# Kernel tuning notes

Hardware: AMD Instinct MI355X
Metric: run time of the kernel (lower is better)

The kernel has to match this reference:

```python
import jax, jax.numpy as jnp
import numpy as np

N_FEAT = 1024
NEG_INF = -1e30  # stand-in for -inf that is safe in fp32 softmax


def setup_inputs() -> dict:
    key = jax.random.key(0)
    k1, k2 = jax.random.split(key)
    T, C = 4096, N_FEAT
    x = jax.random.normal(k1, (T, C), dtype=jnp.float32)
    W = jax.random.normal(k2, (C, 3 * C), dtype=jnp.float32) * (1.0 / np.sqrt(C))
    b = jnp.zeros((3 * C,), dtype=jnp.float32)
    return {"x": x, "W": W, "b": b, "n_padd": 0}


def reference(x, W, b, n_padd):
    T, C = x.shape
    qkv = x @ W + b                      # [T, 3C]
    q, k, v = jnp.split(qkv, 3, axis=1)  # each [T, C]
    att = (q @ k.T) * (1.0 / jnp.sqrt(jnp.float32(C)))  # [T, T]
    idx = jnp.arange(T)
    # causal mask AND padding mask: only keys >= n_padd for queries >= n_padd
    mask = (idx[None, :] <= idx[:, None]) & (idx[None, :] >= n_padd) & (idx[:, None] >= n_padd)
    att = jnp.where(mask, att, NEG_INF)
    att = jax.nn.softmax(att, axis=-1)
    y = att @ v                          # [T, C]
    return y
```

## Files before the change

### kernel.cpp

```cpp
#include <hip/hip_runtime.h>
#include <hip/hip_bf16.h>
#include <math.h>

#define C_DIM 1024
#define QKS  2048

typedef __attribute__((ext_vector_type(8))) short bf16x8;
typedef __attribute__((ext_vector_type(4))) float f32x4;

__device__ __forceinline__ unsigned short f2bf(float f) {
  __hip_bfloat16 h = __float2bfloat16(f);
  return *(reinterpret_cast<unsigned short*>(&h));
}
__device__ __forceinline__ float bf2f(unsigned short u) {
  return __uint_as_float(((unsigned int)u) << 16);
}
__device__ __forceinline__ f32x4 mfma16(bf16x8 a, bf16x8 b, f32x4 c) {
  return __builtin_amdgcn_mfma_f32_16x16x32_bf16(a, b, c, 0, 0, 0);
}
__device__ __forceinline__ void gload_lds16(const unsigned short* g,
                                            unsigned short* l) {
  __builtin_amdgcn_global_load_lds(
      (const __attribute__((address_space(1))) void*)(g),
      (__attribute__((address_space(3))) void*)(l), 16, 0, 0);
}

#define VMCNT(n)  asm volatile("s_waitcnt vmcnt(" #n ")" ::: "memory")
#define LGKMCNT0  asm volatile("s_waitcnt lgkmcnt(0)" ::: "memory")
#define SBAR      __builtin_amdgcn_sched_barrier(0)
#define BARRIER   __builtin_amdgcn_s_barrier()

__global__ __launch_bounds__(256) void prep(
    const float* __restrict__ x, const float* __restrict__ W,
    unsigned short* __restrict__ xb, unsigned short* __restrict__ WT, int nc) {
  __shared__ float Ls[64][65];
  const int id = (int)blockIdx.x;
  if (id < nc) {
    const int i = (id * 256 + threadIdx.x) << 2;
    float4 v = *(const float4*)(x + i);
    ushort4 u;
    u.x = f2bf(v.x); u.y = f2bf(v.y); u.z = f2bf(v.z); u.w = f2bf(v.w);
    *(ushort4*)(xb + i) = u;
    return;
  }
  const int id2 = id - nc;
  const int n0 = (id2 % 48) * 64;
  const int k0 = (id2 / 48) * 64;
  const int c = (threadIdx.x & 15) << 2;
  const int r = threadIdx.x >> 4;
#pragma unroll
  for (int rr = 0; rr < 64; rr += 16) {
    float4 v = *(const float4*)(W + (size_t)(k0 + r + rr) * 3072 + n0 + c);
    Ls[r + rr][c + 0] = v.x; Ls[r + rr][c + 1] = v.y;
    Ls[r + rr][c + 2] = v.z; Ls[r + rr][c + 3] = v.w;
  }
  __syncthreads();
#pragma unroll
  for (int rr = 0; rr < 64; rr += 16) {
    const int X = r + rr;
    ushort4 u;
    u.x = f2bf(Ls[c + 0][X]); u.y = f2bf(Ls[c + 1][X]);
    u.z = f2bf(Ls[c + 2][X]); u.w = f2bf(Ls[c + 3][X]);
    *(ushort4*)(WT + (size_t)(n0 + X) * C_DIM + k0 + c) = u;
  }
}

template <int MODE>
__global__ __launch_bounds__(512) void gemm256(
    const unsigned short* __restrict__ A_, const unsigned short* __restrict__ BT_,
    void* __restrict__ Cv, const float* __restrict__ bias_,
    int lda, int ldb, int ldc, int T) {
  __shared__ __align__(16) unsigned short As[2][2][128][64];
  __shared__ __align__(16) unsigned short Bs[2][2][128][64];

  const int tid = threadIdx.x, lane = tid & 63, w = tid >> 6;
  const int wr = w >> 2, wc = w & 3;
  const int qd = lane >> 4, n16 = lane & 15;

  const unsigned short* A  = A_;
  const unsigned short* BT = BT_;
  const float* bias = bias_;
  unsigned short* Cb = (unsigned short*)Cv;
  float* Cf = (float*)Cv;
  int ldc_ = ldc;
  int m0, n0, kbeg = 0, kend = C_DIM;
  bool use_atomic = false, rowbias = false;

  if (MODE == 4) {
    const int nQKx = QKS >> 8;
    const int nQK  = (T >> 8) * nQKx;
    int id = (int)blockIdx.x;
    if (id < nQK) {
      m0 = (id / nQKx) << 8; n0 = (id % nQKx) << 8;
    } else {
      id -= nQK;
      const int nVx = T >> 8;
      m0 = (id / nVx) << 8; n0 = (id % nVx) << 8;
      A  = BT_ + (size_t)QKS * C_DIM;
      BT = A_;
      Cb = (unsigned short*)Cv + (size_t)T * QKS;
      bias = bias_ + QKS; rowbias = true; ldc_ = T;
    }
  } else if (MODE == 2) {
    if ((int)blockIdx.x > (int)blockIdx.y) return;
    m0 = (int)blockIdx.y << 8; n0 = (int)blockIdx.x << 8;
  } else {
    const int nnx = C_DIM >> 8;
    int id = (int)blockIdx.x;
    const int nx = id % nnx;
    int s = id / nnx;
    int bi = 0;
    while (s >= ((bi >> 2) + 1)) { s -= (bi >> 2) + 1; ++bi; }
    m0 = bi << 8; n0 = nx << 8;
    kbeg = s << 10;
    const int kfull = (bi + 1) << 8;
    kend = kbeg + 1024 < kfull ? kbeg + 1024 : kfull;
    use_atomic = (kfull > 1024);
  }

  const int NT = (kend - kbeg) >> 6;

  const int l3 = lane >> 3;
  const int su = (((lane & 7) ^ l3) << 3);
  const unsigned short* asrc[2][2];
  const unsigned short* bsrc[2][2];
#pragma unroll
  for (int g = 0; g < 2; ++g)
#pragma unroll
    for (int c = 0; c < 2; ++c) {
      asrc[g][c] = A  + (size_t)(m0 + c * 128 + g * 64 + (w << 3) + l3) * lda + kbeg + su;
      bsrc[g][c] = BT + (size_t)(n0 + (c * 2 + (w >> 2)) * 64 + g * 32 + ((w & 3) << 3) + l3) * ldb + kbeg + su;
    }

#define STAGE_A(buf, g, kk) do { \
    gload_lds16(asrc[g][0] + (kk), &As[buf][g][(w << 3)][0]);      \
    gload_lds16(asrc[g][1] + (kk), &As[buf][g][64 + (w << 3)][0]); \
  } while (0)
#define STAGE_B(buf, g, kk) do { \
    gload_lds16(bsrc[g][0] + (kk), &Bs[buf][g][(w << 3)][0]);      \
    gload_lds16(bsrc[g][1] + (kk), &Bs[buf][g][64 + (w << 3)][0]); \
  } while (0)

  const int arow = (wr << 6) + n16;
  const int brow = (wc << 5) + n16;
  const int sw0 = ((qd ^ (n16 & 7)) << 3);
  const int sw1 = (((4 + qd) ^ (n16 & 7)) << 3);

#define READ_A(AA, mh, buf) do { \
  _Pragma("unroll") for (int fm = 0; fm < 4; ++fm) { \
    AA[fm][0] = *(const bf16x8*)&As[buf][mh][arow + fm * 16][sw0]; \
    AA[fm][1] = *(const bf16x8*)&As[buf][mh][arow + fm * 16][sw1]; \
  } } while (0)
#define READ_B(BB, g, buf) do { \
  _Pragma("unroll") for (int fn = 0; fn < 2; ++fn) { \
    BB[fn][0] = *(const bf16x8*)&Bs[buf][g][brow + fn * 16][sw0]; \
    BB[fn][1] = *(const bf16x8*)&Bs[buf][g][brow + fn * 16][sw1]; \
  } } while (0)

  f32x4 acc[8][4];
#pragma unroll
  for (int i = 0; i < 8; ++i)
#pragma unroll
    for (int j = 0; j < 4; ++j) acc[i][j] = (f32x4){0.f, 0.f, 0.f, 0.f};

#define MFMA_QUAD(mh, nh, AA, BB) do { \
  _Pragma("unroll") for (int fm = 0; fm < 4; ++fm) \
  _Pragma("unroll") for (int fn = 0; fn < 2; ++fn) { \
    acc[(mh) * 4 + fm][(nh) * 2 + fn] = mfma16(AA[fm][0], BB[fn][0], acc[(mh) * 4 + fm][(nh) * 2 + fn]); \
    acc[(mh) * 4 + fm][(nh) * 2 + fn] = mfma16(AA[fm][1], BB[fn][1], acc[(mh) * 4 + fm][(nh) * 2 + fn]); \
  } } while (0)

  STAGE_A(0, 0, 0); STAGE_B(0, 0, 0);
  STAGE_A(0, 1, 0); STAGE_B(0, 1, 0);
  if (NT > 1) { STAGE_A(1, 0, 64); STAGE_B(1, 0, 64); }
  if (NT > 1) VMCNT(8); else VMCNT(4);
  SBAR; BARRIER;

  bf16x8 a[4][2], b0[2][2], b1[2][2];
  for (int t = 0; t < NT; ++t) {
    const int p = t & 1, pn = p ^ 1;
    const int knx  = (t + 1) << 6;
    const int knx2 = (t + 2) << 6;
    const bool s1 = (t + 1 < NT), s2 = (t + 2 < NT);

    READ_A(a, 0, p); READ_B(b0, 0, p);
    if (s1) STAGE_A(pn, 1, knx);
    if (s1) { VMCNT(6); } else { VMCNT(0); }
    SBAR; BARRIER; LGKMCNT0; SBAR;
    __builtin_amdgcn_s_setprio(1); MFMA_QUAD(0, 0, a, b0); __builtin_amdgcn_s_setprio(0);
    SBAR; BARRIER;
    READ_B(b1, 1, p);
    if (s1) STAGE_B(pn, 1, knx);
    SBAR; BARRIER; LGKMCNT0; SBAR;
    __builtin_amdgcn_s_setprio(1); MFMA_QUAD(0, 1, a, b1); __builtin_amdgcn_s_setprio(0);
    SBAR; BARRIER;
    READ_A(a, 1, p);
    if (s2) STAGE_A(p, 0, knx2);
    SBAR; BARRIER; LGKMCNT0; SBAR;
    __builtin_amdgcn_s_setprio(1); MFMA_QUAD(1, 0, a, b0); __builtin_amdgcn_s_setprio(0);
    SBAR; BARRIER;
    if (s2) STAGE_B(p, 0, knx2);
    if (s1) { if (s2) { VMCNT(8); } else { VMCNT(4); } }
    SBAR; BARRIER;
    __builtin_amdgcn_s_setprio(1); MFMA_QUAD(1, 1, a, b1); __builtin_amdgcn_s_setprio(0);
    SBAR; BARRIER;
  }

  if (MODE == 3) {
#pragma unroll
    for (int fm = 0; fm < 8; ++fm)
#pragma unroll
      for (int fn = 0; fn < 4; ++fn) {
        const int col  = n0 + (wc << 6) + (fn << 4) + n16;
        const int rowb = m0 + (wr << 7) + (fm << 4) + (qd << 2);
#pragma unroll
        for (int r = 0; r < 4; ++r) {
          if (use_atomic) atomicAdd(&Cf[(size_t)(rowb + r) * ldc_ + col], acc[fm][fn][r]);
          else            Cf[(size_t)(rowb + r) * ldc_ + col] = acc[fm][fn][r];
        }
      }
  } else {
#pragma unroll
    for (int fm = 0; fm < 8; ++fm)
#pragma unroll
      for (int fn = 0; fn < 4; ++fn) {
        const int col  = n0 + (wc << 6) + (fn << 4) + n16;
        const int rowb = m0 + (wr << 7) + (fm << 4) + (qd << 2);
        const float bc = (MODE == 4 && !rowbias) ? bias[col] : 0.f;
#pragma unroll
        for (int r = 0; r < 4; ++r) {
          float v = acc[fm][fn][r];
          if (MODE == 4) v += rowbias ? bias[rowb + r] : bc;
          if (MODE == 2) v *= 0.03125f;
          Cb[(size_t)(rowb + r) * ldc_ + col] = f2bf(v);
        }
      }
  }
#undef STAGE_A
#undef STAGE_B
#undef READ_A
#undef READ_B
#undef MFMA_QUAD
}

__global__ __launch_bounds__(256) void softmax_rows(
    unsigned short* __restrict__ P, const int* __restrict__ np_p, int T,
    float* __restrict__ out) {
  __shared__ float red[8];
  {
    const int nz4 = ((T - 1024) * C_DIM) >> 2;
    const int gidx = (int)blockIdx.x * 256 + threadIdx.x;
    const int stride = (int)gridDim.x * 256;
    const float4 z4 = {0.f, 0.f, 0.f, 0.f};
    for (int i = gidx; i < nz4; i += stride)
      *(float4*)(out + (size_t)1024 * C_DIM + ((size_t)i << 2)) = z4;
  }
  const int i = blockIdx.x;
  const int np = *np_p;
  const int klen = ((i >> 8) + 1) << 8;
  const int tid = threadIdx.x, lane = tid & 63, w = tid >> 6;
  const int j0 = tid << 4;
  unsigned short* rowp = P + (size_t)i * T;
  const bool act = j0 < klen;

  if (i < np) {
    if (act) {
      uint4 z = {0, 0, 0, 0};
      *(uint4*)(rowp + j0) = z;
      *(uint4*)(rowp + j0 + 8) = z;
    }
    return;
  }

  float v[16];
  float mx = -3.0e38f;
  if (act) {
    uint4 u0 = *(const uint4*)(rowp + j0);
    uint4 u1 = *(const uint4*)(rowp + j0 + 8);
    const unsigned int uu[8] = {u0.x, u0.y, u0.z, u0.w, u1.x, u1.y, u1.z, u1.w};
#pragma unroll
    for (int u = 0; u < 8; ++u) {
      v[2 * u]     = bf2f(uu[u] & 0xffff);
      v[2 * u + 1] = bf2f(uu[u] >> 16);
    }
#pragma unroll
    for (int u = 0; u < 16; ++u) {
      const int j = j0 + u;
      if (j > i || j < np) v[u] = -3.0e38f;
      mx = fmaxf(mx, v[u]);
    }
  }
  mx = fmaxf(mx, __shfl_xor(mx, 32));
  mx = fmaxf(mx, __shfl_xor(mx, 16));
  mx = fmaxf(mx, __shfl_xor(mx, 8));
  mx = fmaxf(mx, __shfl_xor(mx, 4));
  mx = fmaxf(mx, __shfl_xor(mx, 2));
  mx = fmaxf(mx, __shfl_xor(mx, 1));
  if (lane == 0) red[w] = mx;
  __syncthreads();
  const float M = fmaxf(fmaxf(red[0], red[1]), fmaxf(red[2], red[3]));

  float sum = 0.f;
  if (act) {
#pragma unroll
    for (int u = 0; u < 16; ++u) {
      const float p = (v[u] > -1.0e30f) ? __expf(v[u] - M) : 0.f;
      v[u] = p;
      sum += p;
    }
  }
  sum += __shfl_xor(sum, 32);
  sum += __shfl_xor(sum, 16);
  sum += __shfl_xor(sum, 8);
  sum += __shfl_xor(sum, 4);
  sum += __shfl_xor(sum, 2);
  sum += __shfl_xor(sum, 1);
  if (lane == 0) red[4 + w] = sum;
  __syncthreads();
  const float inv = 1.0f / (red[4] + red[5] + red[6] + red[7]);

  if (act) {
    unsigned int o[8];
#pragma unroll
    for (int u = 0; u < 8; ++u) {
      const unsigned int lo = f2bf(v[2 * u] * inv);
      const unsigned int hi = f2bf(v[2 * u + 1] * inv);
      o[u] = lo | (hi << 16);
    }
    uint4 s0 = {o[0], o[1], o[2], o[3]};
    uint4 s1 = {o[4], o[5], o[6], o[7]};
    *(uint4*)(rowp + j0) = s0;
    *(uint4*)(rowp + j0 + 8) = s1;
  }
}

__global__ __launch_bounds__(256) void padfix(
    const unsigned short* __restrict__ vtb, const int* __restrict__ np_p,
    float* __restrict__ out, int T) {
  const int np = *np_p;
  const int row0 = blockIdx.x * 32;
  if (row0 >= np) return;
  const int pc = min(np - row0, 32);
  const int c4 = threadIdx.x << 2;
  float a[4] = {0.f, 0.f, 0.f, 0.f};
#pragma unroll
  for (int c = 0; c < 4; ++c) {
    const unsigned short* vr = vtb + (size_t)(c4 + c) * T;
    for (int j = 0; j < T; j += 8) {
      uint4 v = *(const uint4*)(vr + j);
      a[c] += bf2f(v.x & 0xffff) + bf2f(v.x >> 16) + bf2f(v.y & 0xffff) + bf2f(v.y >> 16)
            + bf2f(v.z & 0xffff) + bf2f(v.z >> 16) + bf2f(v.w & 0xffff) + bf2f(v.w >> 16);
    }
  }
  const float inv = 1.0f / (float)T;
  float4 rv = {a[0] * inv, a[1] * inv, a[2] * inv, a[3] * inv};
  for (int r = 0; r < pc; ++r)
    *(float4*)(out + (size_t)(row0 + r) * C_DIM + c4) = rv;
}

extern "C" void kernel_launch(void* const* d_in, const int* in_sizes, int n_in,
                              void* d_out, int out_size, void* d_ws, size_t ws_size,
                              hipStream_t stream) {
  const float* x    = (const float*)d_in[0];
  const float* W    = (const float*)d_in[1];
  const float* b    = (const float*)d_in[2];
  const int* n_padd = (const int*)d_in[3];
  float* out = (float*)d_out;

  const int T = in_sizes[0] / C_DIM;
  unsigned short* qkb = (unsigned short*)d_ws;
  unsigned short* vtb = qkb + (size_t)T * QKS;
  unsigned short* xb  = vtb + (size_t)C_DIM * T;
  unsigned short* WT  = xb  + (size_t)T * C_DIM;
  unsigned short* P   = xb;

  const int nc = (T * C_DIM) >> 10;
  prep<<<nc + 768, 256, 0, stream>>>(x, W, xb, WT, nc);

  {
    const int nQK = (T >> 8) * (QKS >> 8);
    const int nV  = (C_DIM >> 8) * (T >> 8);
    gemm256<4><<<nQK + nV, 512, 0, stream>>>(
        xb, WT, qkb, b, C_DIM, C_DIM, QKS, T);
  }
  gemm256<2><<<dim3(T >> 8, T >> 8), 512, 0, stream>>>(
      qkb, qkb + C_DIM, P, b, QKS, QKS, T, T);
  softmax_rows<<<T, 256, 0, stream>>>(P, n_padd, T, out);
  {
    const int nyt = T >> 8;
    int slots = 0;
    for (int bi = 0; bi < nyt; ++bi) slots += (bi >> 2) + 1;
    gemm256<3><<<slots * (C_DIM >> 8), 512, 0, stream>>>(
        P, vtb, out, b, T, T, C_DIM, T);
  }
  padfix<<<T / 32, 256, 0, stream>>>(vtb, n_padd, out, T);
}
```

Baseline: 221.0 us.

## Rebalance split-K for causal PV GEMM and move output zeroing into QKV GEMM

```diff
diff --git a/kernel.cpp b/kernel.cpp
--- a/kernel.cpp
+++ b/kernel.cpp
@@ -69,7 +69,7 @@
 __global__ __launch_bounds__(512) void gemm256(
     const unsigned short* __restrict__ A_, const unsigned short* __restrict__ BT_,
     void* __restrict__ Cv, const float* __restrict__ bias_,
-    int lda, int ldb, int ldc, int T) {
+    int lda, int ldb, int ldc, int T, float* __restrict__ zout) {
   __shared__ __align__(16) unsigned short As[2][2][128][64];
   __shared__ __align__(16) unsigned short Bs[2][2][128][64];
 
@@ -89,7 +89,17 @@
   if (MODE == 4) {
     const int nQKx = QKS >> 8;
     const int nQK  = (T >> 8) * nQKx;
+    const int nV   = (C_DIM >> 8) * (T >> 8);
     int id = (int)blockIdx.x;
+    if (id >= nQK + nV) {
+      const int zb = id - (nQK + nV);
+      const int ZB = (int)gridDim.x - (nQK + nV);
+      const int n4 = ((T - 512) * C_DIM) >> 2;
+      const float4 z = {0.f, 0.f, 0.f, 0.f};
+      for (int i = zb * 512 + tid; i < n4; i += ZB * 512)
+        *(float4*)(zout + (size_t)512 * C_DIM + ((size_t)i << 2)) = z;
+      return;
+    }
     if (id < nQK) {
       m0 = (id / nQKx) << 8; n0 = (id % nQKx) << 8;
     } else {
@@ -105,17 +115,22 @@
     if ((int)blockIdx.x > (int)blockIdx.y) return;
     m0 = (int)blockIdx.y << 8; n0 = (int)blockIdx.x << 8;
   } else {
-    const int nnx = C_DIM >> 8;
     int id = (int)blockIdx.x;
-    const int nx = id % nnx;
-    int s = id / nnx;
-    int bi = 0;
-    while (s >= ((bi >> 2) + 1)) { s -= (bi >> 2) + 1; ++bi; }
+    int bi = 0, nloc = 1, units = 4;
+    for (;; ++bi) {
+      units = (bi + 1) << 2;
+      nloc  = (units + 9) / 10;
+      const int span = nloc << 2;
+      if (id < span) break;
+      id -= span;
+    }
+    const int nx = id & 3, ch = id >> 2;
+    const int base = units / nloc, rem = units % nloc;
+    const int u0 = ch * base + (ch < rem ? ch : rem);
+    const int u1 = u0 + base + (ch < rem ? 1 : 0);
     m0 = bi << 8; n0 = nx << 8;
-    kbeg = s << 10;
-    const int kfull = (bi + 1) << 8;
-    kend = kbeg + 1024 < kfull ? kbeg + 1024 : kfull;
-    use_atomic = (kfull > 1024);
+    kbeg = u0 << 6; kend = u1 << 6;
+    use_atomic = (nloc > 1);
   }
 
   const int NT = (kend - kbeg) >> 6;
@@ -244,17 +259,8 @@
 }
 
 __global__ __launch_bounds__(256) void softmax_rows(
-    unsigned short* __restrict__ P, const int* __restrict__ np_p, int T,
-    float* __restrict__ out) {
+    unsigned short* __restrict__ P, const int* __restrict__ np_p, int T) {
   __shared__ float red[8];
-  {
-    const int nz4 = ((T - 1024) * C_DIM) >> 2;
-    const int gidx = (int)blockIdx.x * 256 + threadIdx.x;
-    const int stride = (int)gridDim.x * 256;
-    const float4 z4 = {0.f, 0.f, 0.f, 0.f};
-    for (int i = gidx; i < nz4; i += stride)
-      *(float4*)(out + (size_t)1024 * C_DIM + ((size_t)i << 2)) = z4;
-  }
   const int i = blockIdx.x;
   const int np = *np_p;
   const int klen = ((i >> 8) + 1) << 8;
@@ -380,18 +386,22 @@
   {
     const int nQK = (T >> 8) * (QKS >> 8);
     const int nV  = (C_DIM >> 8) * (T >> 8);
-    gemm256<4><<<nQK + nV, 512, 0, stream>>>(
-        xb, WT, qkb, b, C_DIM, C_DIM, QKS, T);
+    int grid = nQK + nV + 64;
+    gemm256<4><<<grid, 512, 0, stream>>>(
+        xb, WT, qkb, b, C_DIM, C_DIM, QKS, T, out);
   }
   gemm256<2><<<dim3(T >> 8, T >> 8), 512, 0, stream>>>(
-      qkb, qkb + C_DIM, P, b, QKS, QKS, T, T);
-  softmax_rows<<<T, 256, 0, stream>>>(P, n_padd, T, out);
+      qkb, qkb + C_DIM, P, b, QKS, QKS, T, T, nullptr);
+  softmax_rows<<<T, 256, 0, stream>>>(P, n_padd, T);
   {
     const int nyt = T >> 8;
     int slots = 0;
-    for (int bi = 0; bi < nyt; ++bi) slots += (bi >> 2) + 1;
-    gemm256<3><<<slots * (C_DIM >> 8), 512, 0, stream>>>(
-        P, vtb, out, b, T, T, C_DIM, T);
+    for (int bi = 0; bi < nyt; ++bi) {
+      const int units = (bi + 1) << 2;
+      slots += ((units + 9) / 10) << 2;
+    }
+    gemm256<3><<<slots, 512, 0, stream>>>(
+        P, vtb, out, b, T, T, C_DIM, T, nullptr);
   }
   padfix<<<T / 32, 256, 0, stream>>>(vtb, n_padd, out, T);
 }
```

Result: slower. 231.8 us (+4.9%).
